# Performance work log

Measured on AMD Instinct MI355X. Metric: run time of the kernel, lower is better.

The kernel has to match this reference:

```python
import jax, jax.numpy as jnp
import numpy as np

NEG_BIG = -9e15

def setup_inputs() -> dict:
    key = jax.random.key(0)
    k1, k2, k3, k4 = jax.random.split(key, 4)
    N, Fin, Fout = 8192, 128, 64
    x = jax.random.normal(k1, (N, Fin), dtype=jnp.float32)
    adj = jax.random.randint(k2, (N, N), 0, 2).astype(jnp.float32)
    W = jax.random.normal(k3, (Fin, Fout), dtype=jnp.float32) * (1.0 / np.sqrt(Fin))
    a = jax.random.normal(k4, (2 * Fout, 1), dtype=jnp.float32) * (1.0 / np.sqrt(2 * Fout))
    return {"x": x, "adj": adj, "W": W, "a": a}

def reference(x, adj, W, a):
    Fout = W.shape[1]
    Wh = x @ W                              # [N, Fout]
    Wh1 = Wh @ a[:Fout, :]                  # [N, 1]
    Wh2 = Wh @ a[Fout:, :]                  # [N, 1]
    e = jax.nn.leaky_relu(Wh1 + Wh2.T, negative_slope=0.2)  # [N, N]
    attention = jnp.where(adj > 0, e, NEG_BIG)
    attention = jax.nn.softmax(attention, axis=1)
    # dropout is identity in eval mode (training=False)
    h_prime = attention @ Wh                # [N, Fout]
    return jax.nn.elu(h_prime)
```

## Files before the change

kernel.cpp:

```cpp
#include <hip/hip_runtime.h>
#include <cstdint>
#include <cstddef>


#define NN   8192
#define FIN  128
#define FOUT 64
#define SJ   8
#define JCHUNK (NN / SJ)

typedef __attribute__((ext_vector_type(8))) short   short8;
typedef __attribute__((ext_vector_type(4))) float   f32x4;

#define LOG2E 1.44269504088896340736f

__global__ __launch_bounds__(256) void gat_phaseA(
    const float* __restrict__ x, const float* __restrict__ W,
    const float* __restrict__ a, unsigned short* __restrict__ Whbt,
    float* __restrict__ Wh1, float* __restrict__ Wh2)
{
  const int wid  = threadIdx.x >> 6;
  const int lane = threadIdx.x & 63;
  const int row0 = (blockIdx.x * 4 + wid) * 4;
  const float a1 = a[lane];
  const float a2 = a[FOUT + lane];
  float acc[4] = {0.f, 0.f, 0.f, 0.f};
#pragma unroll 4
  for (int k = 0; k < FIN; k += 4) {
    float4 wv0 = make_float4(W[(k+0)*FOUT + lane], W[(k+1)*FOUT + lane],
                             W[(k+2)*FOUT + lane], W[(k+3)*FOUT + lane]);
#pragma unroll
    for (int r = 0; r < 4; ++r) {
      float4 xv = *(const float4*)(x + (row0 + r) * FIN + k);
      acc[r] = fmaf(xv.x, wv0.x, acc[r]);
      acc[r] = fmaf(xv.y, wv0.y, acc[r]);
      acc[r] = fmaf(xv.z, wv0.z, acc[r]);
      acc[r] = fmaf(xv.w, wv0.w, acc[r]);
    }
  }
#pragma unroll
  for (int r = 0; r < 4; ++r) {
    unsigned int u = __float_as_uint(acc[r]);
    unsigned int rb = (u + 0x7FFFu + ((u >> 16) & 1u)) >> 16;
    Whbt[lane * NN + row0 + r] = (unsigned short)rb;
    float s1 = acc[r] * a1, s2 = acc[r] * a2;
#pragma unroll
    for (int off = 32; off; off >>= 1) {
      s1 += __shfl_xor(s1, off);
      s2 += __shfl_xor(s2, off);
    }
    if (lane == 0) { Wh1[row0 + r] = s1 * LOG2E; Wh2[row0 + r] = s2 * LOG2E; }
  }
}

__global__ __launch_bounds__(256, 4) void gat_phaseB(
    const float* __restrict__ adj, const unsigned short* __restrict__ Whbt,
    const float* __restrict__ Wh1, const float* __restrict__ Wh2,
    float* __restrict__ accbuf, float* __restrict__ denbuf, int nslices)
{
  const int wid  = threadIdx.x >> 6;
  const int lane = threadIdx.x & 63;
  const int task = blockIdx.x * 4 + wid;
  const int rowTile = task / SJ;
  const int jc      = task % SJ;
  const int m = lane & 15;
  const int q = lane >> 4;
  const int row = rowTile * 16 + m;
  const float wh1 = Wh1[row];
  const float* adjrow = adj + (size_t)row * NN;
  const unsigned short* bbase = Whbt + m * NN;

  f32x4 c0 = {0.f,0.f,0.f,0.f}, c1 = c0, c2 = c0, c3 = c0;
  float rsum = 0.f;

  const int jbeg = jc * JCHUNK;
  const int jend = jbeg + JCHUNK;
  f32x4 ad0 = __builtin_nontemporal_load((const f32x4*)(adjrow + jbeg + q * 8));
  f32x4 ad1 = __builtin_nontemporal_load((const f32x4*)(adjrow + jbeg + q * 8 + 4));

  for (int jb = jbeg; jb < jend; jb += 32) {
    const int j0 = jb + q * 8;
    const int jn = (jb + 32 < jend) ? (j0 + 32) : (jbeg + q * 8);
    f32x4 nd0 = __builtin_nontemporal_load((const f32x4*)(adjrow + jn));
    f32x4 nd1 = __builtin_nontemporal_load((const f32x4*)(adjrow + jn + 4));

    f32x4 w20 = *(const f32x4*)(Wh2 + j0);
    f32x4 w21 = *(const f32x4*)(Wh2 + j0 + 4);
    short8 af;
#pragma unroll
    for (int e = 0; e < 4; ++e) {
      {
        float t = wh1 + w20[e];
        t = fmaxf(t, 0.2f * t);
        float p = exp2f(t) * ad0[e];
        unsigned int pu = __float_as_uint(p) & 0xFFFF0000u;
        rsum += __uint_as_float(pu);
        af[e] = (short)(pu >> 16);
      }
      {
        float t = wh1 + w21[e];
        t = fmaxf(t, 0.2f * t);
        float p = exp2f(t) * ad1[e];
        unsigned int pu = __float_as_uint(p) & 0xFFFF0000u;
        rsum += __uint_as_float(pu);
        af[4 + e] = (short)(pu >> 16);
      }
    }
    const unsigned short* bp = bbase + j0;
    c0 = __builtin_amdgcn_mfma_f32_16x16x32_bf16(af, *(const short8*)(bp          ), c0, 0, 0, 0);
    c1 = __builtin_amdgcn_mfma_f32_16x16x32_bf16(af, *(const short8*)(bp + 16 * NN), c1, 0, 0, 0);
    c2 = __builtin_amdgcn_mfma_f32_16x16x32_bf16(af, *(const short8*)(bp + 32 * NN), c2, 0, 0, 0);
    c3 = __builtin_amdgcn_mfma_f32_16x16x32_bf16(af, *(const short8*)(bp + 48 * NN), c3, 0, 0, 0);

    ad0 = nd0; ad1 = nd1;
  }

  rsum += __shfl_xor(rsum, 16);
  rsum += __shfl_xor(rsum, 32);

  const int slice = (nslices > 1) ? jc : 0;
  float* accout = accbuf + (size_t)slice * (NN * FOUT);
  float* denout = denbuf + slice * NN;
  f32x4 cc[4] = {c0, c1, c2, c3};
  if (nslices > 1) {
    if (q == 0) denout[row] = rsum;
#pragma unroll
    for (int ft = 0; ft < 4; ++ft)
#pragma unroll
      for (int r = 0; r < 4; ++r)
        accout[(rowTile * 16 + q * 4 + r) * FOUT + ft * 16 + m] = cc[ft][r];
  } else {
    if (q == 0) atomicAdd(&denout[row], rsum);
#pragma unroll
    for (int ft = 0; ft < 4; ++ft)
#pragma unroll
      for (int r = 0; r < 4; ++r)
        atomicAdd(&accout[(rowTile * 16 + q * 4 + r) * FOUT + ft * 16 + m], cc[ft][r]);
  }
}

__global__ __launch_bounds__(256) void gat_phaseC(
    const float* __restrict__ accbuf, const float* __restrict__ denbuf,
    float* __restrict__ out, int nslices)
{
  const int idx4 = blockIdx.x * 256 + threadIdx.x;
  const int idx  = idx4 * 4;
  const int row  = idx >> 6;
  f32x4 s = {0.f, 0.f, 0.f, 0.f};
  float d = 0.f;
  for (int sl = 0; sl < nslices; ++sl) {
    f32x4 v = *(const f32x4*)(accbuf + (size_t)sl * (NN * FOUT) + idx);
    s += v;
    d += denbuf[sl * NN + row];
  }
  float inv = 1.0f / d;
  f32x4 o;
#pragma unroll
  for (int e = 0; e < 4; ++e) {
    float v = s[e] * inv;
    o[e] = (v > 0.f) ? v : expm1f(v);
  }
  *(f32x4*)(out + idx) = o;
}

extern "C" void kernel_launch(void* const* d_in, const int* in_sizes, int n_in,
                              void* d_out, int out_size, void* d_ws, size_t ws_size,
                              hipStream_t stream)
{
  const float* x   = (const float*)d_in[0];
  const float* adj = (const float*)d_in[1];
  const float* W   = (const float*)d_in[2];
  const float* a   = (const float*)d_in[3];
  float* out = (float*)d_out;

  const size_t accEl = (size_t)NN * FOUT;
  const size_t roomyBytes = (size_t)SJ * accEl * 4 + (size_t)SJ * NN * 4
                          + (size_t)NN * 8 + (size_t)FOUT * NN * 2;
  const int nslices = (ws_size >= roomyBytes) ? SJ : 1;

  char* ws = (char*)d_ws;
  float* accbuf = (float*)ws;
  size_t off = (size_t)nslices * accEl * 4;
  float* denbuf = (float*)(ws + off); off += (size_t)nslices * NN * 4;
  float* Wh1 = (float*)(ws + off);    off += (size_t)NN * 4;
  float* Wh2 = (float*)(ws + off);    off += (size_t)NN * 4;
  unsigned short* Whbt = (unsigned short*)(ws + off);

  if (nslices == 1)
    hipMemsetAsync(accbuf, 0, accEl * 4 + (size_t)NN * 4, stream);

  gat_phaseA<<<NN / 16, 256, 0, stream>>>(x, W, a, Whbt, Wh1, Wh2);
  gat_phaseB<<<(512 * SJ) / 4, 256, 0, stream>>>(adj, Whbt, Wh1, Wh2,
                                                 accbuf, denbuf, nslices);
  gat_phaseC<<<(NN * FOUT) / 4 / 256, 256, 0, stream>>>(accbuf, denbuf, out, nslices);
}
```

Measured before the change: 437.1 us.

## Software-pipeline phaseB loads and compute row sums with an extra MFMA

Restructures the phaseB inner loop into a fully unrolled, double-buffered pipeline. Wh2 and Whbt B-fragments are prefetched one step ahead and adj two steps ahead, to hide global load latency behind the exp/MFMA work. The per-lane scalar rowsum and its cross-lane shuffles are replaced by a fifth MFMA against a vector of bf16 ones, which moves the denominator onto the matrix unit. The bf16 conversion is now a plain truncation without masking. This raises register pressure under the 4-waves launch bound and adds one MFMA per step.

```diff
diff --git a/kernel.cpp b/kernel.cpp
--- a/kernel.cpp
+++ b/kernel.cpp
@@ -53,6 +53,36 @@
   }
 }
 
+#define GAT_BODY(AD0, AD1, W2C0, W2C1, BC0, BC1, BC2, BC3,                    \
+                 W2N0, W2N1, BN0, BN1, BN2, BN3, JN1, JN2)                    \
+  {                                                                           \
+    W2N0 = *(const f32x4*)(w2base + (JN1));                                   \
+    W2N1 = *(const f32x4*)(w2base + (JN1) + 4);                               \
+    BN0  = *(const short8*)(bbase + (JN1));                                   \
+    BN1  = *(const short8*)(bbase + (JN1) + 16 * NN);                         \
+    BN2  = *(const short8*)(bbase + (JN1) + 32 * NN);                         \
+    BN3  = *(const short8*)(bbase + (JN1) + 48 * NN);                         \
+    short8 af;                                                                \
+    _Pragma("unroll")                                                         \
+    for (int e = 0; e < 4; ++e) {                                             \
+      float t0 = wh1 + (W2C0)[e];                                             \
+      t0 = fmaxf(t0, 0.2f * t0);                   \
+      float p0 = exp2f(t0) * (AD0)[e];              \
+      af[e] = (short)(__float_as_uint(p0) >> 16);          \
+      float t1 = wh1 + (W2C1)[e];                                             \
+      t1 = fmaxf(t1, 0.2f * t1);                                              \
+      float p1 = exp2f(t1) * (AD1)[e];                                        \
+      af[4 + e] = (short)(__float_as_uint(p1) >> 16);                         \
+    }                                                                         \
+    AD0 = __builtin_nontemporal_load((const f32x4*)(adjrow + (JN2)));         \
+    AD1 = __builtin_nontemporal_load((const f32x4*)(adjrow + (JN2) + 4));     \
+    c0 = __builtin_amdgcn_mfma_f32_16x16x32_bf16(af, BC0,  c0, 0, 0, 0);      \
+    c1 = __builtin_amdgcn_mfma_f32_16x16x32_bf16(af, BC1,  c1, 0, 0, 0);      \
+    c2 = __builtin_amdgcn_mfma_f32_16x16x32_bf16(af, BC2,  c2, 0, 0, 0);      \
+    c3 = __builtin_amdgcn_mfma_f32_16x16x32_bf16(af, BC3,  c3, 0, 0, 0);      \
+    c4 = __builtin_amdgcn_mfma_f32_16x16x32_bf16(af, ones, c4, 0, 0, 0);      \
+  }
+
 __global__ __launch_bounds__(256, 4) void gat_phaseB(
     const float* __restrict__ adj, const unsigned short* __restrict__ Whbt,
     const float* __restrict__ Wh1, const float* __restrict__ Wh2,
@@ -67,70 +97,65 @@
   const int q = lane >> 4;
   const int row = rowTile * 16 + m;
   const float wh1 = Wh1[row];
-  const float* adjrow = adj + (size_t)row * NN;
-  const unsigned short* bbase = Whbt + m * NN;
-
-  f32x4 c0 = {0.f,0.f,0.f,0.f}, c1 = c0, c2 = c0, c3 = c0;
-  float rsum = 0.f;
+  const float* adjrow          = adj  + (size_t)row * NN + q * 8;
+  const unsigned short* bbase  = Whbt + m * NN + q * 8;
+  const float* w2base          = Wh2  + q * 8;
+
+  f32x4 c0 = {0.f,0.f,0.f,0.f}, c1 = c0, c2 = c0, c3 = c0, c4 = c0;
+  short8 ones;
+#pragma unroll
+  for (int e = 0; e < 8; ++e) ones[e] = (short)0x3F80;
 
   const int jbeg = jc * JCHUNK;
-  const int jend = jbeg + JCHUNK;
-  f32x4 ad0 = __builtin_nontemporal_load((const f32x4*)(adjrow + jbeg + q * 8));
-  f32x4 ad1 = __builtin_nontemporal_load((const f32x4*)(adjrow + jbeg + q * 8 + 4));
-
-  for (int jb = jbeg; jb < jend; jb += 32) {
-    const int j0 = jb + q * 8;
-    const int jn = (jb + 32 < jend) ? (j0 + 32) : (jbeg + q * 8);
-    f32x4 nd0 = __builtin_nontemporal_load((const f32x4*)(adjrow + jn));
-    f32x4 nd1 = __builtin_nontemporal_load((const f32x4*)(adjrow + jn + 4));
-
-    f32x4 w20 = *(const f32x4*)(Wh2 + j0);
-    f32x4 w21 = *(const f32x4*)(Wh2 + j0 + 4);
-    short8 af;
-#pragma unroll
-    for (int e = 0; e < 4; ++e) {
-      {
-        float t = wh1 + w20[e];
-        t = fmaxf(t, 0.2f * t);
-        float p = exp2f(t) * ad0[e];
-        unsigned int pu = __float_as_uint(p) & 0xFFFF0000u;
-        rsum += __uint_as_float(pu);
-        af[e] = (short)(pu >> 16);
-      }
-      {
-        float t = wh1 + w21[e];
-        t = fmaxf(t, 0.2f * t);
-        float p = exp2f(t) * ad1[e];
-        unsigned int pu = __float_as_uint(p) & 0xFFFF0000u;
-        rsum += __uint_as_float(pu);
-        af[4 + e] = (short)(pu >> 16);
-      }
-    }
-    const unsigned short* bp = bbase + j0;
-    c0 = __builtin_amdgcn_mfma_f32_16x16x32_bf16(af, *(const short8*)(bp          ), c0, 0, 0, 0);
-    c1 = __builtin_amdgcn_mfma_f32_16x16x32_bf16(af, *(const short8*)(bp + 16 * NN), c1, 0, 0, 0);
-    c2 = __builtin_amdgcn_mfma_f32_16x16x32_bf16(af, *(const short8*)(bp + 32 * NN), c2, 0, 0, 0);
-    c3 = __builtin_amdgcn_mfma_f32_16x16x32_bf16(af, *(const short8*)(bp + 48 * NN), c3, 0, 0, 0);
-
-    ad0 = nd0; ad1 = nd1;
-  }
-
-  rsum += __shfl_xor(rsum, 16);
-  rsum += __shfl_xor(rsum, 32);
+
+  f32x4 adA0, adA1, adB0, adB1;
+  f32x4 w2A0, w2A1, w2B0, w2B1;
+  short8 bA0, bA1, bA2, bA3, bB0, bB1, bB2, bB3;
+
+  w2A0 = *(const f32x4*)(w2base + jbeg);
+  w2A1 = *(const f32x4*)(w2base + jbeg + 4);
+  bA0  = *(const short8*)(bbase + jbeg);
+  bA1  = *(const short8*)(bbase + jbeg + 16 * NN);
+  bA2  = *(const short8*)(bbase + jbeg + 32 * NN);
+  bA3  = *(const short8*)(bbase + jbeg + 48 * NN);
+  adA0 = __builtin_nontemporal_load((const f32x4*)(adjrow + jbeg));
+  adA1 = __builtin_nontemporal_load((const f32x4*)(adjrow + jbeg + 4));
+  adB0 = __builtin_nontemporal_load((const f32x4*)(adjrow + jbeg + 32));
+  adB1 = __builtin_nontemporal_load((const f32x4*)(adjrow + jbeg + 36));
+
+#pragma unroll
+  for (int bb = 0; bb < 32; bb += 2) {
+    const int jE = bb * 32;
+    const int j1 = (bb + 1 < 32) ? jE + 32 : 0;
+    const int j2 = (bb + 2 < 32) ? jE + 64 : 0;
+    const int j3 = (bb + 3 < 32) ? jE + 96 : 0;
+    GAT_BODY(adA0, adA1, w2A0, w2A1, bA0, bA1, bA2, bA3,
+             w2B0, w2B1, bB0, bB1, bB2, bB3, jbeg + j1, jbeg + j2);
+    GAT_BODY(adB0, adB1, w2B0, w2B1, bB0, bB1, bB2, bB3,
+             w2A0, w2A1, bA0, bA1, bA2, bA3, jbeg + j2, jbeg + j3);
+  }
 
   const int slice = (nslices > 1) ? jc : 0;
   float* accout = accbuf + (size_t)slice * (NN * FOUT);
   float* denout = denbuf + slice * NN;
   f32x4 cc[4] = {c0, c1, c2, c3};
   if (nslices > 1) {
-    if (q == 0) denout[row] = rsum;
+    if (m == 0) {
+#pragma unroll
+      for (int r = 0; r < 4; ++r)
+        denout[rowTile * 16 + q * 4 + r] = c4[r];
+    }
 #pragma unroll
     for (int ft = 0; ft < 4; ++ft)
 #pragma unroll
       for (int r = 0; r < 4; ++r)
         accout[(rowTile * 16 + q * 4 + r) * FOUT + ft * 16 + m] = cc[ft][r];
   } else {
-    if (q == 0) atomicAdd(&denout[row], rsum);
+    if (m == 0) {
+#pragma unroll
+      for (int r = 0; r < 4; ++r)
+        atomicAdd(&denout[rowTile * 16 + q * 4 + r], c4[r]);
+    }
 #pragma unroll
     for (int ft = 0; ft < 4; ++ft)
 #pragma unroll
```

After: 426.7 us. 1.02x faster.

## Stage adj tiles through swizzled LDS with coalesced row loads and prefetch

Applied to the files above, without the earlier changes.

Phase B now loads adj in a coalesced pattern, where each group of 16 lanes reads 256 contiguous bytes of one row, instead of each lane reading 32 bytes at a scattered row position. Each wave writes these tiles to a per-wave, XOR-swizzled, double-buffered LDS region and reads them back in the MFMA operand layout. Loads are software-pipelined one 128-column tile ahead, with sched_barriers to pin the ordering, and the B operands and Wh2 for two k-steps are batched. The aim is better DRAM coalescing and more memory-level parallelism on the dominant adj stream, at the cost of 32KB LDS per block, more registers, and extra LDS traffic.

```diff
diff --git a/kernel.cpp b/kernel.cpp
--- a/kernel.cpp
+++ b/kernel.cpp
@@ -13,6 +13,7 @@
 typedef __attribute__((ext_vector_type(4))) float   f32x4;
 
 #define LOG2E 1.44269504088896340736f
+#define NTL(p) __builtin_nontemporal_load((const f32x4*)(p))
 
 __global__ __launch_bounds__(256) void gat_phaseA(
     const float* __restrict__ x, const float* __restrict__ W,
@@ -53,6 +54,67 @@
   }
 }
 
+#define AF_MFMA(AD0, AD1, W20, W21, B0, B1, B2, B3)                      \
+  {                                                                      \
+    short8 af;                                                           \
+    _Pragma("unroll")                                                    \
+    for (int e = 0; e < 4; ++e) {                                        \
+      float t0 = wh1 + (W20)[e];                                         \
+      t0 = fmaxf(t0, 0.2f * t0);              \
+      float p0 = exp2f(t0) * (AD0)[e];         \
+      unsigned int pu0 = __float_as_uint(p0) & 0xFFFF0000u;              \
+      rsum += __uint_as_float(pu0);          \
+      af[e] = (short)(pu0 >> 16);                                        \
+      float t1 = wh1 + (W21)[e];                                         \
+      t1 = fmaxf(t1, 0.2f * t1);                                         \
+      float p1 = exp2f(t1) * (AD1)[e];                                   \
+      unsigned int pu1 = __float_as_uint(p1) & 0xFFFF0000u;              \
+      rsum += __uint_as_float(pu1);                                      \
+      af[4 + e] = (short)(pu1 >> 16);                                    \
+    }                                                                    \
+    c0 = __builtin_amdgcn_mfma_f32_16x16x32_bf16(af, B0, c0, 0, 0, 0);   \
+    c1 = __builtin_amdgcn_mfma_f32_16x16x32_bf16(af, B1, c1, 0, 0, 0);   \
+    c2 = __builtin_amdgcn_mfma_f32_16x16x32_bf16(af, B2, c2, 0, 0, 0);   \
+    c3 = __builtin_amdgcn_mfma_f32_16x16x32_bf16(af, B3, c3, 0, 0, 0);   \
+  }
+
+#define BLOCKC(BUF, BOFF, W20, W21, B0, B1, B2, B3)                      \
+  {                                                                      \
+    f32x4 ad0 = *(const f32x4*)((BUF) + rA + (BOFF));                    \
+    f32x4 ad1 = *(const f32x4*)((BUF) + rB + (BOFF));                    \
+    AF_MFMA(ad0, ad1, W20, W21, B0, B1, B2, B3)                          \
+  }
+
+#define TILE_SECTION(ST0, ST1, ST2, ST3, BUF, JB, SOFF, PF)              \
+  {                                                                      \
+    *(f32x4*)((BUF) + w0       ) = ST0;                                  \
+    *(f32x4*)((BUF) + w1       ) = ST1;                                  \
+    *(f32x4*)((BUF) + w0 + 2048) = ST2;                                  \
+    *(f32x4*)((BUF) + w1 + 2048) = ST3;                                  \
+    const float* w2p = Wh2 + (JB) + q * 8;                               \
+    f32x4 w20a = *(const f32x4*)(w2p);                                   \
+    f32x4 w21a = *(const f32x4*)(w2p + 4);                               \
+    f32x4 w20b = *(const f32x4*)(w2p + 32);                              \
+    f32x4 w21b = *(const f32x4*)(w2p + 36);                              \
+    const unsigned short* bp = bbase + (JB);                             \
+    short8 ba0 = *(const short8*)(bp);                                   \
+    short8 ba1 = *(const short8*)(bp + 16 * NN);                         \
+    short8 ba2 = *(const short8*)(bp + 32 * NN);                         \
+    short8 ba3 = *(const short8*)(bp + 48 * NN);                         \
+    short8 bb0 = *(const short8*)(bp + 32);                              \
+    short8 bb1 = *(const short8*)(bp + 32 + 16 * NN);                    \
+    short8 bb2 = *(const short8*)(bp + 32 + 32 * NN);                    \
+    short8 bb3 = *(const short8*)(bp + 32 + 48 * NN);                    \
+    __builtin_amdgcn_sched_barrier(0);                                   \
+    if (PF) {                                                            \
+      ST0 = NTL(s0 + (SOFF)); ST1 = NTL(s1 + (SOFF));                    \
+      ST2 = NTL(s2 + (SOFF)); ST3 = NTL(s3 + (SOFF));                    \
+    }                                                                    \
+    __builtin_amdgcn_sched_barrier(0);                                   \
+    BLOCKC(BUF, 0,   w20a, w21a, ba0, ba1, ba2, ba3);                    \
+    BLOCKC(BUF, 128, w20b, w21b, bb0, bb1, bb2, bb3);                    \
+  }
+
 __global__ __launch_bounds__(256, 4) void gat_phaseB(
     const float* __restrict__ adj, const unsigned short* __restrict__ Whbt,
     const float* __restrict__ Wh1, const float* __restrict__ Wh2,
@@ -67,52 +129,41 @@
   const int q = lane >> 4;
   const int row = rowTile * 16 + m;
   const float wh1 = Wh1[row];
-  const float* adjrow = adj + (size_t)row * NN;
-  const unsigned short* bbase = Whbt + m * NN;
+  const unsigned short* bbase = Whbt + m * NN + q * 8;
+  const int jbeg = jc * JCHUNK;
+
+  __shared__ __align__(16) char ldsmem[4][2][4096];
+  char* buf0 = &ldsmem[wid][0][0];
+  char* buf1 = &ldsmem[wid][1][0];
+
+  const int r4 = lane >> 4;
+  const int xw = (lane & 15) * 16;
+  const int mw0 = r4, mw1 = 4 + r4;
+  const int w0 = mw0 * 256 + (xw ^ ((mw0 & 7) << 4));
+  const int w1 = mw1 * 256 + (xw ^ ((mw1 & 7) << 4));
+  const int sw = (m & 7) << 4;
+  const int rA = m * 256 + ((q * 32) ^ sw);
+  const int rB = rA ^ 16;
+
+  const char* s0 = (const char*)adj
+                 + ((size_t)(rowTile * 16 + r4) * NN + jbeg) * 4 + xw;
+  const char* s1 = s0 + (size_t)4  * NN * 4;
+  const char* s2 = s0 + (size_t)8  * NN * 4;
+  const char* s3 = s0 + (size_t)12 * NN * 4;
 
   f32x4 c0 = {0.f,0.f,0.f,0.f}, c1 = c0, c2 = c0, c3 = c0;
   float rsum = 0.f;
 
-  const int jbeg = jc * JCHUNK;
-  const int jend = jbeg + JCHUNK;
-  f32x4 ad0 = __builtin_nontemporal_load((const f32x4*)(adjrow + jbeg + q * 8));
-  f32x4 ad1 = __builtin_nontemporal_load((const f32x4*)(adjrow + jbeg + q * 8 + 4));
-
-  for (int jb = jbeg; jb < jend; jb += 32) {
-    const int j0 = jb + q * 8;
-    const int jn = (jb + 32 < jend) ? (j0 + 32) : (jbeg + q * 8);
-    f32x4 nd0 = __builtin_nontemporal_load((const f32x4*)(adjrow + jn));
-    f32x4 nd1 = __builtin_nontemporal_load((const f32x4*)(adjrow + jn + 4));
-
-    f32x4 w20 = *(const f32x4*)(Wh2 + j0);
-    f32x4 w21 = *(const f32x4*)(Wh2 + j0 + 4);
-    short8 af;
-#pragma unroll
-    for (int e = 0; e < 4; ++e) {
-      {
-        float t = wh1 + w20[e];
-        t = fmaxf(t, 0.2f * t);
-        float p = exp2f(t) * ad0[e];
-        unsigned int pu = __float_as_uint(p) & 0xFFFF0000u;
-        rsum += __uint_as_float(pu);
-        af[e] = (short)(pu >> 16);
-      }
-      {
-        float t = wh1 + w21[e];
-        t = fmaxf(t, 0.2f * t);
-        float p = exp2f(t) * ad1[e];
-        unsigned int pu = __float_as_uint(p) & 0xFFFF0000u;
-        rsum += __uint_as_float(pu);
-        af[4 + e] = (short)(pu >> 16);
-      }
-    }
-    const unsigned short* bp = bbase + j0;
-    c0 = __builtin_amdgcn_mfma_f32_16x16x32_bf16(af, *(const short8*)(bp          ), c0, 0, 0, 0);
-    c1 = __builtin_amdgcn_mfma_f32_16x16x32_bf16(af, *(const short8*)(bp + 16 * NN), c1, 0, 0, 0);
-    c2 = __builtin_amdgcn_mfma_f32_16x16x32_bf16(af, *(const short8*)(bp + 32 * NN), c2, 0, 0, 0);
-    c3 = __builtin_amdgcn_mfma_f32_16x16x32_bf16(af, *(const short8*)(bp + 48 * NN), c3, 0, 0, 0);
-
-    ad0 = nd0; ad1 = nd1;
+  f32x4 stA0 = NTL(s0),       stA1 = NTL(s1),       stA2 = NTL(s2),       stA3 = NTL(s3);
+  f32x4 stB0 = NTL(s0 + 256), stB1 = NTL(s1 + 256), stB2 = NTL(s2 + 256), stB3 = NTL(s3 + 256);
+  s0 += 512; s1 += 512; s2 += 512; s3 += 512;
+
+  for (int tt = 0; tt < 8; ++tt) {
+    const int JB0 = jbeg + tt * 128;
+    const bool pf = (tt < 7);
+    TILE_SECTION(stA0, stA1, stA2, stA3, buf0, JB0,      0,   pf);
+    TILE_SECTION(stB0, stB1, stB2, stB3, buf1, JB0 + 64, 256, pf);
+    s0 += 512; s1 += 512; s2 += 512; s3 += 512;
   }
 
   rsum += __shfl_xor(rsum, 16);
```

New measurement: 430.1 us. Within noise of the previous version (-1.6%).

## Process two row tiles per wave with double-buffered B and adj prefetch

Applied to the files above, without the earlier changes.

Each wave now handles 32 rows (two 16-row tiles) so the Wh2 and bf16 Wh B-fragment loads are shared across both tiles. The j loop is fully unrolled with ping-pong registers that prefetch the next B, Wh2 and adj data one step ahead, and adj two steps ahead. SJ goes from 8 to 16 to keep the grid size unchanged, and launch bounds drop to 3 waves-per-EU minimum to make room for the extra registers. The cost is higher register pressure and lower occupancy, plus twice as many partial slices for phase C to reduce, which also enlarges the workspace needed for the multi-slice path.

```diff
diff --git a/kernel.cpp b/kernel.cpp
--- a/kernel.cpp
+++ b/kernel.cpp
@@ -6,13 +6,14 @@
 #define NN   8192
 #define FIN  128
 #define FOUT 64
-#define SJ   8
+#define SJ   16
 #define JCHUNK (NN / SJ)
 
 typedef __attribute__((ext_vector_type(8))) short   short8;
 typedef __attribute__((ext_vector_type(4))) float   f32x4;
 
 #define LOG2E 1.44269504088896340736f
+#define NTL(p) __builtin_nontemporal_load((const f32x4*)(p))
 
 __global__ __launch_bounds__(256) void gat_phaseA(
     const float* __restrict__ x, const float* __restrict__ W,
@@ -53,7 +54,48 @@
   }
 }
 
-__global__ __launch_bounds__(256, 4) void gat_phaseB(
+#define AF_ONE(AF, AD0, AD1, W20, W21, WH1, RS)                          \
+    _Pragma("unroll")                                                    \
+    for (int e = 0; e < 4; ++e) {                                        \
+      float t0 = (WH1) + (W20)[e];                                       \
+      t0 = fmaxf(t0, 0.2f * t0);              \
+      float p0 = exp2f(t0) * (AD0)[e];         \
+      unsigned int pu0 = __float_as_uint(p0) & 0xFFFF0000u;              \
+      RS += __uint_as_float(pu0);            \
+      AF[e] = (short)(pu0 >> 16);                                        \
+      float t1 = (WH1) + (W21)[e];                                       \
+      t1 = fmaxf(t1, 0.2f * t1);                                         \
+      float p1 = exp2f(t1) * (AD1)[e];                                   \
+      unsigned int pu1 = __float_as_uint(p1) & 0xFFFF0000u;              \
+      RS += __uint_as_float(pu1);                                        \
+      AF[4 + e] = (short)(pu1 >> 16);                                    \
+    }
+
+#define GAT_BODY(AD00, AD01, AD10, AD11, W2C0, W2C1, BC0, BC1, BC2, BC3, \
+                 W2N0, W2N1, BN0, BN1, BN2, BN3, JN1, JN2)               \
+  {                                                                      \
+    W2N0 = *(const f32x4*)(w2base + (JN1));                              \
+    W2N1 = *(const f32x4*)(w2base + (JN1) + 4);                          \
+    BN0  = *(const short8*)(bbase + (JN1));                              \
+    BN1  = *(const short8*)(bbase + (JN1) + 16 * NN);                    \
+    BN2  = *(const short8*)(bbase + (JN1) + 32 * NN);                    \
+    BN3  = *(const short8*)(bbase + (JN1) + 48 * NN);                    \
+    short8 af0, af1;                                                     \
+    AF_ONE(af0, AD00, AD01, W2C0, W2C1, wh1_0, rsum0);                   \
+    AF_ONE(af1, AD10, AD11, W2C0, W2C1, wh1_1, rsum1);                   \
+    AD00 = NTL(adjrow0 + (JN2)); AD01 = NTL(adjrow0 + (JN2) + 4);        \
+    AD10 = NTL(adjrow1 + (JN2)); AD11 = NTL(adjrow1 + (JN2) + 4);        \
+    c00 = __builtin_amdgcn_mfma_f32_16x16x32_bf16(af0, BC0, c00, 0,0,0); \
+    c01 = __builtin_amdgcn_mfma_f32_16x16x32_bf16(af0, BC1, c01, 0,0,0); \
+    c02 = __builtin_amdgcn_mfma_f32_16x16x32_bf16(af0, BC2, c02, 0,0,0); \
+    c03 = __builtin_amdgcn_mfma_f32_16x16x32_bf16(af0, BC3, c03, 0,0,0); \
+    c10 = __builtin_amdgcn_mfma_f32_16x16x32_bf16(af1, BC0, c10, 0,0,0); \
+    c11 = __builtin_amdgcn_mfma_f32_16x16x32_bf16(af1, BC1, c11, 0,0,0); \
+    c12 = __builtin_amdgcn_mfma_f32_16x16x32_bf16(af1, BC2, c12, 0,0,0); \
+    c13 = __builtin_amdgcn_mfma_f32_16x16x32_bf16(af1, BC3, c13, 0,0,0); \
+  }
+
+__global__ __launch_bounds__(256, 3) void gat_phaseB(
     const float* __restrict__ adj, const unsigned short* __restrict__ Whbt,
     const float* __restrict__ Wh1, const float* __restrict__ Wh2,
     float* __restrict__ accbuf, float* __restrict__ denbuf, int nslices)
@@ -61,81 +103,80 @@
   const int wid  = threadIdx.x >> 6;
   const int lane = threadIdx.x & 63;
   const int task = blockIdx.x * 4 + wid;
-  const int rowTile = task / SJ;
-  const int jc      = task % SJ;
+  const int rg   = task / SJ;
+  const int jc   = task % SJ;
   const int m = lane & 15;
   const int q = lane >> 4;
-  const int row = rowTile * 16 + m;
-  const float wh1 = Wh1[row];
-  const float* adjrow = adj + (size_t)row * NN;
-  const unsigned short* bbase = Whbt + m * NN;
-
-  f32x4 c0 = {0.f,0.f,0.f,0.f}, c1 = c0, c2 = c0, c3 = c0;
-  float rsum = 0.f;
+  const int r0 = rg * 32 + m;
+  const int r1 = r0 + 16;
+  const float wh1_0 = Wh1[r0];
+  const float wh1_1 = Wh1[r1];
+  const float* adjrow0 = adj + (size_t)r0 * NN + q * 8;
+  const float* adjrow1 = adj + (size_t)r1 * NN + q * 8;
+  const unsigned short* bbase = Whbt + m * NN + q * 8;
+  const float* w2base = Wh2 + q * 8;
+
+  f32x4 c00 = {0.f,0.f,0.f,0.f}, c01 = c00, c02 = c00, c03 = c00;
+  f32x4 c10 = c00, c11 = c00, c12 = c00, c13 = c00;
+  float rsum0 = 0.f, rsum1 = 0.f;
 
   const int jbeg = jc * JCHUNK;
-  const int jend = jbeg + JCHUNK;
-  f32x4 ad0 = __builtin_nontemporal_load((const f32x4*)(adjrow + jbeg + q * 8));
-  f32x4 ad1 = __builtin_nontemporal_load((const f32x4*)(adjrow + jbeg + q * 8 + 4));
-
-  for (int jb = jbeg; jb < jend; jb += 32) {
-    const int j0 = jb + q * 8;
-    const int jn = (jb + 32 < jend) ? (j0 + 32) : (jbeg + q * 8);
-    f32x4 nd0 = __builtin_nontemporal_load((const f32x4*)(adjrow + jn));
-    f32x4 nd1 = __builtin_nontemporal_load((const f32x4*)(adjrow + jn + 4));
-
-    f32x4 w20 = *(const f32x4*)(Wh2 + j0);
-    f32x4 w21 = *(const f32x4*)(Wh2 + j0 + 4);
-    short8 af;
-#pragma unroll
-    for (int e = 0; e < 4; ++e) {
-      {
-        float t = wh1 + w20[e];
-        t = fmaxf(t, 0.2f * t);
-        float p = exp2f(t) * ad0[e];
-        unsigned int pu = __float_as_uint(p) & 0xFFFF0000u;
-        rsum += __uint_as_float(pu);
-        af[e] = (short)(pu >> 16);
-      }
-      {
-        float t = wh1 + w21[e];
-        t = fmaxf(t, 0.2f * t);
-        float p = exp2f(t) * ad1[e];
-        unsigned int pu = __float_as_uint(p) & 0xFFFF0000u;
-        rsum += __uint_as_float(pu);
-        af[4 + e] = (short)(pu >> 16);
-      }
-    }
-    const unsigned short* bp = bbase + j0;
-    c0 = __builtin_amdgcn_mfma_f32_16x16x32_bf16(af, *(const short8*)(bp          ), c0, 0, 0, 0);
-    c1 = __builtin_amdgcn_mfma_f32_16x16x32_bf16(af, *(const short8*)(bp + 16 * NN), c1, 0, 0, 0);
-    c2 = __builtin_amdgcn_mfma_f32_16x16x32_bf16(af, *(const short8*)(bp + 32 * NN), c2, 0, 0, 0);
-    c3 = __builtin_amdgcn_mfma_f32_16x16x32_bf16(af, *(const short8*)(bp + 48 * NN), c3, 0, 0, 0);
-
-    ad0 = nd0; ad1 = nd1;
-  }
-
-  rsum += __shfl_xor(rsum, 16);
-  rsum += __shfl_xor(rsum, 32);
+
+  f32x4 w2A0, w2A1, w2B0, w2B1;
+  short8 bA0, bA1, bA2, bA3, bB0, bB1, bB2, bB3;
+  f32x4 adA00, adA01, adA10, adA11;
+  f32x4 adB00, adB01, adB10, adB11;
+
+  w2A0 = *(const f32x4*)(w2base + jbeg);
+  w2A1 = *(const f32x4*)(w2base + jbeg + 4);
+  bA0  = *(const short8*)(bbase + jbeg);
+  bA1  = *(const short8*)(bbase + jbeg + 16 * NN);
+  bA2  = *(const short8*)(bbase + jbeg + 32 * NN);
+  bA3  = *(const short8*)(bbase + jbeg + 48 * NN);
+  adA00 = NTL(adjrow0 + jbeg);      adA01 = NTL(adjrow0 + jbeg + 4);
+  adA10 = NTL(adjrow1 + jbeg);      adA11 = NTL(adjrow1 + jbeg + 4);
+  adB00 = NTL(adjrow0 + jbeg + 32); adB01 = NTL(adjrow0 + jbeg + 36);
+  adB10 = NTL(adjrow1 + jbeg + 32); adB11 = NTL(adjrow1 + jbeg + 36);
+
+#pragma unroll
+  for (int bb = 0; bb < 16; bb += 2) {
+    const int j1 = (bb + 1 < 16) ? (bb + 1) * 32 : 0;
+    const int j2 = (bb + 2 < 16) ? (bb + 2) * 32 : 0;
+    const int j3 = (bb + 3 < 16) ? (bb + 3) * 32 : 0;
+    GAT_BODY(adA00, adA01, adA10, adA11, w2A0, w2A1, bA0, bA1, bA2, bA3,
+             w2B0, w2B1, bB0, bB1, bB2, bB3, jbeg + j1, jbeg + j2);
+    GAT_BODY(adB00, adB01, adB10, adB11, w2B0, w2B1, bB0, bB1, bB2, bB3,
+             w2A0, w2A1, bA0, bA1, bA2, bA3, jbeg + j2, jbeg + j3);
+  }
+
+  rsum0 += __shfl_xor(rsum0, 16);
+  rsum0 += __shfl_xor(rsum0, 32);
+  rsum1 += __shfl_xor(rsum1, 16);
+  rsum1 += __shfl_xor(rsum1, 32);
 
   const int slice = (nslices > 1) ? jc : 0;
   float* accout = accbuf + (size_t)slice * (NN * FOUT);
   float* denout = denbuf + slice * NN;
-  f32x4 cc[4] = {c0, c1, c2, c3};
+  f32x4 cc0[4] = {c00, c01, c02, c03};
+  f32x4 cc1[4] = {c10, c11, c12, c13};
   if (nslices > 1) {
-    if (q == 0) denout[row] = rsum;
+    if (q == 0) { denout[r0] = rsum0; denout[r1] = rsum1; }
 #pragma unroll
     for (int ft = 0; ft < 4; ++ft)
 #pragma unroll
-      for (int r = 0; r < 4; ++r)
-        accout[(rowTile * 16 + q * 4 + r) * FOUT + ft * 16 + m] = cc[ft][r];
+      for (int r = 0; r < 4; ++r) {
+        accout[(rg * 32 +      q * 4 + r) * FOUT + ft * 16 + m] = cc0[ft][r];
+        accout[(rg * 32 + 16 + q * 4 + r) * FOUT + ft * 16 + m] = cc1[ft][r];
+      }
   } else {
-    if (q == 0) atomicAdd(&denout[row], rsum);
+    if (q == 0) { atomicAdd(&denout[r0], rsum0); atomicAdd(&denout[r1], rsum1); }
 #pragma unroll
     for (int ft = 0; ft < 4; ++ft)
 #pragma unroll
-      for (int r = 0; r < 4; ++r)
-        atomicAdd(&accout[(rowTile * 16 + q * 4 + r) * FOUT + ft * 16 + m], cc[ft][r]);
+      for (int r = 0; r < 4; ++r) {
+        atomicAdd(&accout[(rg * 32 +      q * 4 + r) * FOUT + ft * 16 + m], cc0[ft][r]);
+        atomicAdd(&accout[(rg * 32 + 16 + q * 4 + r) * FOUT + ft * 16 + m], cc1[ft][r]);
+      }
   }
 }
 
@@ -190,7 +231,7 @@
     hipMemsetAsync(accbuf, 0, accEl * 4 + (size_t)NN * 4, stream);
 
   gat_phaseA<<<NN / 16, 256, 0, stream>>>(x, W, a, Whbt, Wh1, Wh2);
-  gat_phaseB<<<(512 * SJ) / 4, 256, 0, stream>>>(adj, Whbt, Wh1, Wh2,
-                                                 accbuf, denbuf, nslices);
+  gat_phaseB<<<((NN / 32) * SJ) / 4, 256, 0, stream>>>(adj, Whbt, Wh1, Wh2,
+                                                       accbuf, denbuf, nslices);
   gat_phaseC<<<(NN * FOUT) / 4 / 256, 256, 0, stream>>>(accbuf, denbuf, out, nslices);
 }
```

New measurement: 396.0 us. 9.4% less time.
